# Kernel optimization log

Measured on AMD Instinct MI355X. Metric: run time of the kernel, lower is better.

The kernel has to match this reference:

```python
import jax, jax.numpy as jnp
import numpy as np

DOWNSAMPLE = 4
REG = 0.05
SINKHORN_ITERS = 50
LAMBDA_OT = 1.0
LAMBDA_TV = 1.0


def setup_inputs() -> dict:
    key = jax.random.key(0)
    k1, k2 = jax.random.split(key)
    pred = jax.random.uniform(k1, (16, 1, 256, 256), dtype=jnp.float32)
    gt = jax.random.uniform(k2, (16, 1, 256, 256), dtype=jnp.float32)
    return {"pred": pred, "gt": gt, "epoch": 5, "max_epoch": 10}


def _avg_pool(x, k):
    B, C, H, W = x.shape
    return x.reshape(B, C, H // k, k, W // k, k).mean(axis=(3, 5))


def _normalize(x, n):
    # relu then normalize to a distribution; fall back to uniform if sum==0
    x = jnp.maximum(x, 0.0)
    s = x.sum(axis=1, keepdims=True)  # [B,1]
    return jnp.where(s > 0, x / s, jnp.full_like(x, 1.0 / n))


def _curriculum_loss(pred, gt, epoch, max_epoch):
    B = pred.shape[0]
    # --- counting loss: L1 between total counts ---
    pc = pred.reshape(B, -1).sum(axis=1)
    gc = gt.reshape(B, -1).sum(axis=1)
    l_count = jnp.abs(pc - gc).mean()

    t = float(epoch) / float(max(1, max_epoch))
    ot_w = LAMBDA_OT * t
    tv_w = LAMBDA_TV * t

    # --- OT loss (batched Sinkhorn) ---
    pd = _avg_pool(pred, DOWNSAMPLE)
    gd = _avg_pool(gt, DOWNSAMPLE)
    h, w = pd.shape[2], pd.shape[3]
    n = h * w
    ys = jnp.arange(h, dtype=jnp.float32)
    xs = jnp.arange(w, dtype=jnp.float32)
    yy, xx = jnp.meshgrid(ys, xs, indexing="ij")
    yf = yy.reshape(-1)  # [n]
    xf = xx.reshape(-1)
    # squared euclidean cost matrix [n,n], built separably (no [n,n,2] temp)
    M = (yf[:, None] - yf[None, :]) ** 2 + (xf[:, None] - xf[None, :]) ** 2
    K = jnp.exp(-M / REG)  # [n,n]

    a = _normalize(pd.reshape(B, -1), n)  # [B,n]
    b = _normalize(gd.reshape(B, -1), n)

    def step(uv, _):
        u, v = uv
        u = a / (v @ K.T)  # K @ v per sample, batched
        v = b / (u @ K)    # K.T @ u per sample, batched
        return (u, v), None

    ones = jnp.ones((B, n), dtype=pred.dtype)
    (u, v), _ = jax.lax.scan(step, (ones, ones), None, length=SINKHORN_ITERS)
    # cost_b = sum_ij u_i K_ij v_j M_ij
    cost = jnp.einsum("bn,nm,bm->b", u, K * M, v)
    l_ot = cost.mean()

    # --- total variation loss ---
    dx = jnp.abs(pred[:, :, :, 1:] - pred[:, :, :, :-1]).mean()
    dy = jnp.abs(pred[:, :, 1:, :] - pred[:, :, :-1, :]).mean()
    l_tv = dx + dy

    return l_count + ot_w * l_ot + tv_w * l_tv


def reference(pred, gt, epoch, max_epoch):
    return _curriculum_loss(pred, gt, epoch, max_epoch)
```

## Files before the change

kernel.cpp:

```cpp
#include <hip/hip_runtime.h>
#include <math.h>


#define KW1 2.0611536224385578e-09f
#define MW2 8.4967085105831778e-18f
#define RP2 72
#define PDOFF 2048
#define GDOFF 67584

__device__ __forceinline__ float dpp_right(float x) {
  return __int_as_float(__builtin_amdgcn_update_dpp(
      0, __float_as_int(x), 0x101, 0xF, 0xF, true));
}
__device__ __forceinline__ float dpp_left(float x) {
  return __int_as_float(__builtin_amdgcn_update_dpp(
      0, __float_as_int(x), 0x111, 0xF, 0xF, true));
}
__device__ __forceinline__ float wshr1(float x) {
  return __int_as_float(__builtin_amdgcn_update_dpp(
      0, __float_as_int(x), 0x138, 0xF, 0xF, true));
}
__device__ __forceinline__ float wshl1(float x) {
  return __int_as_float(__builtin_amdgcn_update_dpp(
      0, __float_as_int(x), 0x130, 0xF, 0xF, true));
}

__device__ __forceinline__ float ad4(const float4 a, const float4 b) {
  return fabsf(a.x - b.x) + fabsf(a.y - b.y) + fabsf(a.z - b.z) + fabsf(a.w - b.w);
}
__device__ __forceinline__ float agent_ld(const float* p) {
  return __hip_atomic_load(p, __ATOMIC_RELAXED, __HIP_MEMORY_SCOPE_AGENT);
}

__global__ __launch_bounds__(256) void prep_kernel(
    const float* __restrict__ pred, const float* __restrict__ gt,
    float* __restrict__ ws) {
  __shared__ float rbuf[16];
  const int g = blockIdx.x;
  const int im = g >> 4, band = g & 15;
  const int t = threadIdx.x;
  const int ppy = t >> 6, ppx = t & 63;
  const float* pb = pred + im * 65536;
  const float* gb = gt + im * 65536;
  const int sr0 = band * 16 + ppy * 4;
  const int c0 = ppx * 4;

  float4 q[4];
  float ps = 0.f, gs = 0.f, sx = 0.f, sy = 0.f;
#pragma unroll
  for (int r = 0; r < 4; ++r) {
    q[r] = *(const float4*)(pb + (sr0 + r) * 256 + c0);
    const float4 e = *(const float4*)(gb + (sr0 + r) * 256 + c0);
    ps += (q[r].x + q[r].y) + (q[r].z + q[r].w);
    gs += (e.x + e.y) + (e.z + e.w);
    sx += fabsf(q[r].y - q[r].x) + fabsf(q[r].z - q[r].y) + fabsf(q[r].w - q[r].z);
    const float nf = __shfl_down(q[r].x, 1);
    if (ppx < 63) sx += fabsf(nf - q[r].w);
  }
  sy += ad4(q[1], q[0]) + ad4(q[2], q[1]) + ad4(q[3], q[2]);
  if (sr0 + 4 < 256) {
    const float4 qn = *(const float4*)(pb + (sr0 + 4) * 256 + c0);
    sy += ad4(qn, q[3]);
  }
  const int prow = band * 4 + ppy;
  ws[PDOFF + im * 4096 + prow * 64 + ppx] = fmaxf(ps * 0.0625f, 0.f);
  ws[GDOFF + im * 4096 + prow * 64 + ppx] = fmaxf(gs * 0.0625f, 0.f);

  float r0 = ps, r1 = gs, r2 = sx, r3 = sy;
#pragma unroll
  for (int o = 32; o > 0; o >>= 1) {
    r0 += __shfl_down(r0, o); r1 += __shfl_down(r1, o);
    r2 += __shfl_down(r2, o); r3 += __shfl_down(r3, o);
  }
  if ((t & 63) == 0) {
    const int w = t >> 6;
    rbuf[w * 4 + 0] = r0; rbuf[w * 4 + 1] = r1;
    rbuf[w * 4 + 2] = r2; rbuf[w * 4 + 3] = r3;
  }
  __syncthreads();
  if (t == 0) {
    float a0 = 0, a1 = 0, a2 = 0, a3 = 0;
    for (int w = 0; w < 4; ++w) {
      a0 += rbuf[w * 4]; a1 += rbuf[w * 4 + 1];
      a2 += rbuf[w * 4 + 2]; a3 += rbuf[w * 4 + 3];
    }
    ws[g] = a0; ws[256 + g] = a1; ws[512 + g] = a2; ws[768 + g] = a3;
  }
}

__global__ __launch_bounds__(256) void sink_kernel(
    float* __restrict__ ws, const int* __restrict__ epoch,
    const int* __restrict__ max_epoch, float* __restrict__ out,
    unsigned int* __restrict__ cnt) {
  __shared__ float SuL[6 * 64], SuR[6 * 64], SvL[6 * 64], SvR[6 * 64];
  __shared__ float rbuf[24];
  __shared__ int lastflag;

  const int b = blockIdx.x;
  const int t = threadIdx.x;
  const int w = t >> 6;
  const int l = t & 63;

  for (int i = t; i < 6 * 64; i += 256) {
    SuL[i] = 0.f; SuR[i] = 0.f; SvL[i] = 0.f; SvR[i] = 0.f;
  }
  __syncthreads();
  SvL[(w + 1) * 64 + l] = 1.f;
  SvR[(w + 1) * 64 + l] = 1.f;

  float av[16], bv[16];
  {
    const float* P = &ws[PDOFF + b * 4096 + l * 64 + w * 16];
    const float* G = &ws[GDOFF + b * 4096 + l * 64 + w * 16];
    float spd = 0.f, sgd = 0.f;
#pragma unroll
    for (int c4 = 0; c4 < 4; ++c4) {
      const float4 qa = *(const float4*)(P + 4 * c4);
      av[4 * c4] = qa.x; av[4 * c4 + 1] = qa.y;
      av[4 * c4 + 2] = qa.z; av[4 * c4 + 3] = qa.w;
      spd += (qa.x + qa.y) + (qa.z + qa.w);
      const float4 qb = *(const float4*)(G + 4 * c4);
      bv[4 * c4] = qb.x; bv[4 * c4 + 1] = qb.y;
      bv[4 * c4 + 2] = qb.z; bv[4 * c4 + 3] = qb.w;
      sgd += (qb.x + qb.y) + (qb.z + qb.w);
    }
#pragma unroll
    for (int o = 32; o > 0; o >>= 1) {
      spd += __shfl_down(spd, o); sgd += __shfl_down(sgd, o);
    }
    if (l == 0) { rbuf[w * 2] = spd; rbuf[w * 2 + 1] = sgd; }
  }
  __syncthreads();
  const float Sp = rbuf[0] + rbuf[2] + rbuf[4] + rbuf[6];
  const float Sg = rbuf[1] + rbuf[3] + rbuf[5] + rbuf[7];
#pragma unroll
  for (int c = 0; c < 16; ++c) {
    av[c] = (Sp > 0.f) ? (av[c] / Sp) : (1.f / 4096.f);
    bv[c] = (Sg > 0.f) ? (bv[c] / Sg) : (1.f / 4096.f);
  }

  const int rdL = w * 64 + l;
  const int rdR = (w + 2) * 64 + l;
  const int wr  = (w + 1) * 64 + l;

  float uu[16], vv[16], hh[16];
#pragma unroll
  for (int c = 0; c < 16; ++c) vv[c] = 1.f;
  __syncthreads();

#pragma unroll 1
  for (int it = 0; it < 50; ++it) {
    {
      const float xl = SvR[rdL];
      const float xr = SvL[rdR];
      hh[0] = fmaf(KW1, xl + vv[1], vv[0]);
#pragma unroll
      for (int c = 1; c < 15; ++c) hh[c] = fmaf(KW1, vv[c - 1] + vv[c + 1], vv[c]);
      hh[15] = fmaf(KW1, vv[14] + xr, vv[15]);
#pragma unroll
      for (int c = 0; c < 16; ++c) {
        const float up = wshr1(hh[c]);
        const float dn = wshl1(hh[c]);
        uu[c] = av[c] * __builtin_amdgcn_rcpf(fmaf(KW1, up + dn, hh[c]));
      }
      SuL[wr] = uu[0]; SuR[wr] = uu[15];
    }
    __syncthreads();
    {
      const float xl = SuR[rdL];
      const float xr = SuL[rdR];
      hh[0] = fmaf(KW1, xl + uu[1], uu[0]);
#pragma unroll
      for (int c = 1; c < 15; ++c) hh[c] = fmaf(KW1, uu[c - 1] + uu[c + 1], uu[c]);
      hh[15] = fmaf(KW1, uu[14] + xr, uu[15]);
#pragma unroll
      for (int c = 0; c < 16; ++c) {
        const float up = wshr1(hh[c]);
        const float dn = wshl1(hh[c]);
        vv[c] = bv[c] * __builtin_amdgcn_rcpf(fmaf(KW1, up + dn, hh[c]));
      }
      SvL[wr] = vv[0]; SvR[wr] = vv[15];
    }
    __syncthreads();
  }

  float c = 0.f;
  {
    const float xl = SvR[rdL];
    const float xr = SvL[rdR];
#pragma unroll
    for (int cc = 0; cc < 16; ++cc) {
      const float vl = (cc == 0) ? xl : vv[cc - 1];
      const float vr = (cc == 15) ? xr : vv[cc + 1];
      const float s = vl + vr;
      const float e = (wshr1(vv[cc]) + wshl1(vv[cc])) + s;
      const float d = wshr1(s) + wshl1(s);
      c += uu[cc] * fmaf(MW2, d, KW1 * e);
    }
  }
#pragma unroll
  for (int o = 32; o > 0; o >>= 1) c += __shfl_down(c, o);
  if (l == 0) rbuf[8 + w] = c;
  __syncthreads();
  if (t == 0) {
    ws[1024 + b] = rbuf[8] + rbuf[9] + rbuf[10] + rbuf[11];
    __threadfence();
    const unsigned int old = atomicAdd(cnt, 1u);
    lastflag = (old == 15u) ? 1 : 0;
  }
  __syncthreads();

  if (lastflag) {
    __threadfence();
    float myPc = agent_ld(&ws[t]);
    float myGc = agent_ld(&ws[256 + t]);
    float myTx = agent_ld(&ws[512 + t]);
    float myTy = agent_ld(&ws[768 + t]);
#pragma unroll
    for (int o = 8; o > 0; o >>= 1) {
      myPc += __shfl_down(myPc, o, 16);
      myGc += __shfl_down(myGc, o, 16);
    }
    float d = ((t & 15) == 0) ? fabsf(myPc - myGc) : 0.f;
    float ct = (t < 16) ? agent_ld(&ws[1024 + t]) : 0.f;
#pragma unroll
    for (int o = 32; o > 0; o >>= 1) {
      d += __shfl_down(d, o); ct += __shfl_down(ct, o);
      myTx += __shfl_down(myTx, o); myTy += __shfl_down(myTy, o);
    }
    if ((t & 63) == 0) {
      const int ww = t >> 6;
      rbuf[ww * 4] = d; rbuf[ww * 4 + 1] = ct;
      rbuf[ww * 4 + 2] = myTx; rbuf[ww * 4 + 3] = myTy;
    }
    __syncthreads();
    if (t == 0) {
      float lc = 0, lot = 0, tvx = 0, tvy = 0;
      for (int ww = 0; ww < 4; ++ww) {
        lc += rbuf[ww * 4]; lot += rbuf[ww * 4 + 1];
        tvx += rbuf[ww * 4 + 2]; tvy += rbuf[ww * 4 + 3];
      }
      int me = max_epoch[0]; if (me < 1) me = 1;
      const float tt = (float)epoch[0] / (float)me;
      const float ltv = tvx / (16.f * 256.f * 255.f) + tvy / (16.f * 255.f * 256.f);
      out[0] = lc * (1.f / 16.f) + tt * (lot * (1.f / 16.f)) + tt * ltv;
    }
  }
}

#define SPW1 2.0611536224385578e-09f
__device__ __forceinline__ void hrow4(const float f[4], float h[4]) {
  const float l = dpp_left(f[3]);
  const float r = dpp_right(f[0]);
  h[0] = fmaf(KW1, l + f[1], f[0]);
  h[1] = fmaf(KW1, f[0] + f[2], f[1]);
  h[2] = fmaf(KW1, f[1] + f[3], f[2]);
  h[3] = fmaf(KW1, f[2] + r, f[3]);
}
__device__ __forceinline__ void phase_core(
    const float prev[4][4], float ph[4][4],
    const float cf0[4], const float cf3[4],
    float2 mA, float4 mB, float2 mC, float2 pA, float4 pB, float2 pC,
    float* __restrict__ RT_wr, float* __restrict__ RB_wr, int wb,
    float out0[4], float out3[4]) {
  hrow4(prev[0], ph[0]); hrow4(prev[1], ph[1]);
  hrow4(prev[2], ph[2]); hrow4(prev[3], ph[3]);
  float hm[4], hp[4];
  hm[0] = fmaf(KW1, mA.y + mB.y, mB.x);
  hm[1] = fmaf(KW1, mB.x + mB.z, mB.y);
  hm[2] = fmaf(KW1, mB.y + mB.w, mB.z);
  hm[3] = fmaf(KW1, mB.z + mC.x, mB.w);
  hp[0] = fmaf(KW1, pA.y + pB.y, pB.x);
  hp[1] = fmaf(KW1, pB.x + pB.z, pB.y);
  hp[2] = fmaf(KW1, pB.y + pB.w, pB.z);
  hp[3] = fmaf(KW1, pB.z + pC.x, pB.w);
#pragma unroll
  for (int j = 0; j < 4; ++j)
    out0[j] = cf0[j] * __builtin_amdgcn_rcpf(fmaf(KW1, hm[j] + ph[1][j], ph[0][j]));
#pragma unroll
  for (int j = 0; j < 4; ++j)
    out3[j] = cf3[j] * __builtin_amdgcn_rcpf(fmaf(KW1, ph[2][j] + hp[j], ph[3][j]));
  *(float4*)&RT_wr[wb] = make_float4(out0[0], out0[1], out0[2], out0[3]);
  *(float4*)&RB_wr[wb] = make_float4(out3[0], out3[1], out3[2], out3[3]);
}

__global__ __launch_bounds__(256) void fused_fallback(
    const float* __restrict__ pred, const float* __restrict__ gt,
    float* __restrict__ ws, const int* __restrict__ epoch,
    const int* __restrict__ max_epoch, float* __restrict__ out,
    unsigned int* __restrict__ cnt) {
  __shared__ float RTu[18 * RP2], RBu[18 * RP2];
  __shared__ float RTv[18 * RP2], RBv[18 * RP2];
  __shared__ float rbuf[24];

  const int b = blockIdx.x;
  const int t = threadIdx.x;
  const int tyg = t >> 4, tx = t & 15;
  const int y0 = tyg * 4, x0 = tx * 4;

  for (int i = t; i < 18 * RP2; i += 256) {
    RTu[i] = 0.f; RBu[i] = 0.f; RTv[i] = 0.f; RBv[i] = 0.f;
  }

  const float* pb = pred + b * 65536;
  const float* gb = gt + b * 65536;
  const int sr0 = 4 * y0, sc0 = 4 * x0;

  float pd[4][4], gd[4][4];
  float4 pr0, pr1, pr2, pr3;
  float spraw = 0.f, sgraw = 0.f, sx = 0.f, sy = 0.f;
#pragma unroll
  for (int i = 0; i < 4; ++i) {
    float a0 = 0.f, a1 = 0.f, a2 = 0.f, a3 = 0.f;
    float c0 = 0.f, c1 = 0.f, c2 = 0.f, c3 = 0.f;
#pragma unroll 1
    for (int rr = 0; rr < 4; ++rr) {
      const int r = i * 4 + rr;
      const float* prow = pb + (sr0 + r) * 256 + sc0;
      const float4 q0 = *(const float4*)(prow);
      const float4 q1 = *(const float4*)(prow + 4);
      const float4 q2 = *(const float4*)(prow + 8);
      const float4 q3 = *(const float4*)(prow + 12);
      const float s0 = (q0.x + q0.y) + (q0.z + q0.w);
      const float s1 = (q1.x + q1.y) + (q1.z + q1.w);
      const float s2 = (q2.x + q2.y) + (q2.z + q2.w);
      const float s3 = (q3.x + q3.y) + (q3.z + q3.w);
      a0 += s0; a1 += s1; a2 += s2; a3 += s3;
      spraw += (s0 + s1) + (s2 + s3);
      sx += fabsf(q0.y - q0.x) + fabsf(q0.z - q0.y) + fabsf(q0.w - q0.z)
          + fabsf(q1.x - q0.w)
          + fabsf(q1.y - q1.x) + fabsf(q1.z - q1.y) + fabsf(q1.w - q1.z)
          + fabsf(q2.x - q1.w)
          + fabsf(q2.y - q2.x) + fabsf(q2.z - q2.y) + fabsf(q2.w - q2.z)
          + fabsf(q3.x - q2.w)
          + fabsf(q3.y - q3.x) + fabsf(q3.z - q3.y) + fabsf(q3.w - q3.z);
      const float nf = dpp_right(q0.x);
      if (tx < 15) sx += fabsf(nf - q3.w);
      if (r > 0) sy += ad4(q0, pr0) + ad4(q1, pr1) + ad4(q2, pr2) + ad4(q3, pr3);
      pr0 = q0; pr1 = q1; pr2 = q2; pr3 = q3;
      const float* grow = gb + (sr0 + r) * 256 + sc0;
      const float4 g0 = *(const float4*)(grow);
      const float4 g1 = *(const float4*)(grow + 4);
      const float4 g2 = *(const float4*)(grow + 8);
      const float4 g3 = *(const float4*)(grow + 12);
      const float u0 = (g0.x + g0.y) + (g0.z + g0.w);
      const float u1 = (g1.x + g1.y) + (g1.z + g1.w);
      const float u2 = (g2.x + g2.y) + (g2.z + g2.w);
      const float u3 = (g3.x + g3.y) + (g3.z + g3.w);
      c0 += u0; c1 += u1; c2 += u2; c3 += u3;
      sgraw += (u0 + u1) + (u2 + u3);
    }
    pd[i][0] = a0; pd[i][1] = a1; pd[i][2] = a2; pd[i][3] = a3;
    gd[i][0] = c0; gd[i][1] = c1; gd[i][2] = c2; gd[i][3] = c3;
  }
  if (tyg < 15) {
    const float* prow = pb + (sr0 + 16) * 256 + sc0;
    sy += ad4(*(const float4*)(prow), pr0) + ad4(*(const float4*)(prow + 4), pr1)
        + ad4(*(const float4*)(prow + 8), pr2) + ad4(*(const float4*)(prow + 12), pr3);
  }

  float spd = 0.f, sgd = 0.f;
#pragma unroll
  for (int i = 0; i < 4; ++i)
#pragma unroll
    for (int j = 0; j < 4; ++j) {
      pd[i][j] = fmaxf(pd[i][j] * 0.0625f, 0.f); spd += pd[i][j];
      gd[i][j] = fmaxf(gd[i][j] * 0.0625f, 0.f); sgd += gd[i][j];
    }

  float r0 = spraw, r1 = sgraw, r2 = spd, r3 = sgd, r4 = sx, r5 = sy;
#pragma unroll
  for (int o = 32; o > 0; o >>= 1) {
    r0 += __shfl_down(r0, o); r1 += __shfl_down(r1, o);
    r2 += __shfl_down(r2, o); r3 += __shfl_down(r3, o);
    r4 += __shfl_down(r4, o); r5 += __shfl_down(r5, o);
  }
  if ((t & 63) == 0) {
    const int w = t >> 6;
    rbuf[w * 6 + 0] = r0; rbuf[w * 6 + 1] = r1; rbuf[w * 6 + 2] = r2;
    rbuf[w * 6 + 3] = r3; rbuf[w * 6 + 4] = r4; rbuf[w * 6 + 5] = r5;
  }
  __syncthreads();
  if (t == 0) {
    float a0 = 0, a1 = 0, a2 = 0, a3 = 0, a4 = 0, a5 = 0;
    for (int w = 0; w < 4; ++w) {
      a0 += rbuf[w * 6 + 0]; a1 += rbuf[w * 6 + 1]; a2 += rbuf[w * 6 + 2];
      a3 += rbuf[w * 6 + 3]; a4 += rbuf[w * 6 + 4]; a5 += rbuf[w * 6 + 5];
    }
    ws[b] = a0; ws[16 + b] = a1; ws[48 + b] = a4; ws[64 + b] = a5;
    rbuf[0] = a2; rbuf[1] = a3;
  }
  __syncthreads();
  const float Sp = rbuf[0], Sg = rbuf[1];

  float av[4][4], bv[4][4];
#pragma unroll
  for (int i = 0; i < 4; ++i)
#pragma unroll
    for (int j = 0; j < 4; ++j) {
      av[i][j] = (Sp > 0.f) ? (pd[i][j] / Sp) : (1.f / 4096.f);
      bv[i][j] = (Sg > 0.f) ? (gd[i][j] / Sg) : (1.f / 4096.f);
    }

  const int rbb = tyg * RP2 + x0 + 2;
  const int rtb = (tyg + 2) * RP2 + x0 + 2;
  const int wb  = (1 + tyg) * RP2 + 4 + x0;

  float uu[4][4], vv[4][4], uh[4][4], vh[4][4];
#pragma unroll
  for (int i = 0; i < 4; ++i)
#pragma unroll
    for (int j = 0; j < 4; ++j) vv[i][j] = 1.f;
  *(float4*)&RTv[wb] = make_float4(1.f, 1.f, 1.f, 1.f);
  *(float4*)&RBv[wb] = make_float4(1.f, 1.f, 1.f, 1.f);
  __syncthreads();

#pragma unroll 1
  for (int it = 0; it < 50; ++it) {
    {
      const float2 mA = *(const float2*)&RBv[rbb];
      const float4 mB = *(const float4*)&RBv[rbb + 2];
      const float2 mC = *(const float2*)&RBv[rbb + 6];
      const float2 pA = *(const float2*)&RTv[rtb];
      const float4 pB = *(const float4*)&RTv[rtb + 2];
      const float2 pC = *(const float2*)&RTv[rtb + 6];
      if (it != 0) {
#pragma unroll
        for (int j = 0; j < 4; ++j) {
          vv[1][j] = bv[1][j] * __builtin_amdgcn_rcpf(fmaf(KW1, uh[0][j] + uh[2][j], uh[1][j]));
          vv[2][j] = bv[2][j] * __builtin_amdgcn_rcpf(fmaf(KW1, uh[1][j] + uh[3][j], uh[2][j]));
        }
      }
      phase_core(vv, vh, av[0], av[3], mA, mB, mC, pA, pB, pC,
                 RTu, RBu, wb, uu[0], uu[3]);
    }
    __syncthreads();
    {
      const float2 mA = *(const float2*)&RBu[rbb];
      const float4 mB = *(const float4*)&RBu[rbb + 2];
      const float2 mC = *(const float2*)&RBu[rbb + 6];
      const float2 pA = *(const float2*)&RTu[rtb];
      const float4 pB = *(const float4*)&RTu[rtb + 2];
      const float2 pC = *(const float2*)&RTu[rtb + 6];
#pragma unroll
      for (int j = 0; j < 4; ++j) {
        uu[1][j] = av[1][j] * __builtin_amdgcn_rcpf(fmaf(KW1, vh[0][j] + vh[2][j], vh[1][j]));
        uu[2][j] = av[2][j] * __builtin_amdgcn_rcpf(fmaf(KW1, vh[1][j] + vh[3][j], vh[2][j]));
      }
      phase_core(uu, uh, bv[0], bv[3], mA, mB, mC, pA, pB, pC,
                 RTv, RBv, wb, vv[0], vv[3]);
    }
    __syncthreads();
  }
#pragma unroll
  for (int j = 0; j < 4; ++j) {
    vv[1][j] = bv[1][j] * __builtin_amdgcn_rcpf(fmaf(KW1, uh[0][j] + uh[2][j], uh[1][j]));
    vv[2][j] = bv[2][j] * __builtin_amdgcn_rcpf(fmaf(KW1, uh[1][j] + uh[3][j], uh[2][j]));
  }

  float c = 0.f;
  {
    const float2 mA = *(const float2*)&RBv[rbb];
    const float4 mB = *(const float4*)&RBv[rbb + 2];
    const float2 mC = *(const float2*)&RBv[rbb + 6];
    const float2 pA = *(const float2*)&RTv[rtb];
    const float4 pB = *(const float4*)&RTv[rtb + 2];
    const float2 pC = *(const float2*)&RTv[rtb + 6];
    float W[6][6];
    W[0][0] = mA.y; W[0][1] = mB.x; W[0][2] = mB.y;
    W[0][3] = mB.z; W[0][4] = mB.w; W[0][5] = mC.x;
    W[5][0] = pA.y; W[5][1] = pB.x; W[5][2] = pB.y;
    W[5][3] = pB.z; W[5][4] = pB.w; W[5][5] = pC.x;
#pragma unroll
    for (int i = 0; i < 4; ++i) {
      W[1 + i][0] = dpp_left(vv[i][3]);
      W[1 + i][5] = dpp_right(vv[i][0]);
#pragma unroll
      for (int j = 0; j < 4; ++j) W[1 + i][1 + j] = vv[i][j];
    }
#pragma unroll
    for (int i = 0; i < 4; ++i)
#pragma unroll
      for (int j = 0; j < 4; ++j) {
        const float e = (W[i][j + 1] + W[i + 2][j + 1])
                      + (W[i + 1][j] + W[i + 1][j + 2]);
        const float d = (W[i][j] + W[i][j + 2])
                      + (W[i + 2][j] + W[i + 2][j + 2]);
        c += uu[i][j] * fmaf(MW2, d, KW1 * e);
      }
  }
#pragma unroll
  for (int o = 32; o > 0; o >>= 1) c += __shfl_down(c, o);
  if ((t & 63) == 0) rbuf[t >> 6] = c;
  __syncthreads();
  if (t == 0) {
    ws[32 + b] = rbuf[0] + rbuf[1] + rbuf[2] + rbuf[3];
    __threadfence();
    const unsigned int old = atomicAdd(cnt, 1u);
    if (old == 15u) {
      __threadfence();
      float lc = 0.f, lot = 0.f, tvx = 0.f, tvy = 0.f;
      for (int k = 0; k < 16; ++k) {
        const float p = agent_ld(&ws[k]);
        const float g = agent_ld(&ws[16 + k]);
        const float ct = agent_ld(&ws[32 + k]);
        const float x = agent_ld(&ws[48 + k]);
        const float y = agent_ld(&ws[64 + k]);
        lc += fabsf(p - g); lot += ct; tvx += x; tvy += y;
      }
      int me = max_epoch[0]; if (me < 1) me = 1;
      const float tt = (float)epoch[0] / (float)me;
      const float ltv = tvx / (16.f * 256.f * 255.f) + tvy / (16.f * 255.f * 256.f);
      out[0] = lc * (1.f / 16.f) + tt * (lot * (1.f / 16.f)) + tt * ltv;
    }
  }
}

extern "C" void kernel_launch(void* const* d_in, const int* in_sizes, int n_in,
                              void* d_out, int out_size, void* d_ws, size_t ws_size,
                              hipStream_t stream) {
  const float* pred = (const float*)d_in[0];
  const float* gt   = (const float*)d_in[1];
  const int* epoch  = (const int*)d_in[2];
  const int* max_ep = (const int*)d_in[3];
  float* out = (float*)d_out;
  float* ws  = (float*)d_ws;

  if (ws_size >= 600000) {
    unsigned int* cnt = (unsigned int*)((char*)d_ws + 4160);
    hipMemsetAsync(cnt, 0, 4, stream);
    prep_kernel<<<dim3(256), dim3(256), 0, stream>>>(pred, gt, ws);
    sink_kernel<<<dim3(16), dim3(256), 0, stream>>>(ws, epoch, max_ep, out, cnt);
  } else {
    unsigned int* cnt = (unsigned int*)((char*)d_ws + 384);
    hipMemsetAsync(cnt, 0, 4, stream);
    fused_fallback<<<dim3(16), dim3(256), 0, stream>>>(pred, gt, ws, epoch,
                                                       max_ep, out, cnt);
  }
}
```

Before: 103.9 us.

## Use 4-column halos so Sinkhorn waves exchange boundaries every two iterations

Each wave now keeps 24 columns in registers: its own 16 plus a 4-column halo on each side. It runs four half-steps (two Sinkhorn iterations), letting the valid region shrink by one column per half-step, and only then swaps halos through shared memory. That replaces two barriers per iteration with one barrier per two iterations, and the shared buffers are double-buffered so a single sync is enough. The cost is extra redundant arithmetic and more registers per thread, plus a clamp on the denominator to avoid dividing by zero in halo columns outside the field.

```diff
diff --git a/kernel.cpp b/kernel.cpp
--- a/kernel.cpp
+++ b/kernel.cpp
@@ -30,6 +30,20 @@
 }
 __device__ __forceinline__ float agent_ld(const float* p) {
   return __hip_atomic_load(p, __ATOMIC_RELAXED, __HIP_MEMORY_SCOPE_AGENT);
+}
+
+template <int LO, int HI>
+__device__ __forceinline__ void half_phase(const float (&src)[24],
+                                           const float (&cf)[24],
+                                           float (&dst)[24], float (&hh)[24]) {
+#pragma unroll
+  for (int i = LO; i <= HI; ++i)
+    hh[i] = fmaf(KW1, src[i - 1] + src[i + 1], src[i]);
+#pragma unroll
+  for (int i = LO; i <= HI; ++i) {
+    const float d = fmaf(KW1, wshr1(hh[i]) + wshl1(hh[i]), hh[i]);
+    dst[i] = cf[i] * __builtin_amdgcn_rcpf(fmaxf(d, 1e-30f));
+  }
 }
 
 __global__ __launch_bounds__(256) void prep_kernel(
@@ -92,7 +106,7 @@
     float* __restrict__ ws, const int* __restrict__ epoch,
     const int* __restrict__ max_epoch, float* __restrict__ out,
     unsigned int* __restrict__ cnt) {
-  __shared__ float SuL[6 * 64], SuR[6 * 64], SvL[6 * 64], SvR[6 * 64];
+  __shared__ float SL[2][6 * 256], SR[2][6 * 256];
   __shared__ float rbuf[24];
   __shared__ int lastflag;
 
@@ -100,103 +114,76 @@
   const int t = threadIdx.x;
   const int w = t >> 6;
   const int l = t & 63;
-
-  for (int i = t; i < 6 * 64; i += 256) {
-    SuL[i] = 0.f; SuR[i] = 0.f; SvL[i] = 0.f; SvR[i] = 0.f;
-  }
-  __syncthreads();
-  SvL[(w + 1) * 64 + l] = 1.f;
-  SvR[(w + 1) * 64 + l] = 1.f;
-
-  float av[16], bv[16];
-  {
-    const float* P = &ws[PDOFF + b * 4096 + l * 64 + w * 16];
-    const float* G = &ws[GDOFF + b * 4096 + l * 64 + w * 16];
-    float spd = 0.f, sgd = 0.f;
-#pragma unroll
-    for (int c4 = 0; c4 < 4; ++c4) {
-      const float4 qa = *(const float4*)(P + 4 * c4);
-      av[4 * c4] = qa.x; av[4 * c4 + 1] = qa.y;
-      av[4 * c4 + 2] = qa.z; av[4 * c4 + 3] = qa.w;
-      spd += (qa.x + qa.y) + (qa.z + qa.w);
-      const float4 qb = *(const float4*)(G + 4 * c4);
-      bv[4 * c4] = qb.x; bv[4 * c4 + 1] = qb.y;
-      bv[4 * c4 + 2] = qb.z; bv[4 * c4 + 3] = qb.w;
-      sgd += (qb.x + qb.y) + (qb.z + qb.w);
-    }
-#pragma unroll
-    for (int o = 32; o > 0; o >>= 1) {
-      spd += __shfl_down(spd, o); sgd += __shfl_down(sgd, o);
-    }
-    if (l == 0) { rbuf[w * 2] = spd; rbuf[w * 2 + 1] = sgd; }
-  }
+  const int colbase = 16 * w - 4;
+
+  for (int i = t; i < 6 * 256; i += 256) {
+    SL[0][i] = 0.f; SR[0][i] = 0.f; SL[1][i] = 0.f; SR[1][i] = 0.f;
+  }
+
+  float av[24], bv[24];
+  const float* P = &ws[PDOFF + b * 4096 + l * 64];
+  const float* G = &ws[GDOFF + b * 4096 + l * 64];
+#pragma unroll
+  for (int k = 0; k < 6; ++k) {
+    const int c0 = colbase + 4 * k;
+    if (c0 >= 0 && c0 <= 60) {
+      const float4 qa = *(const float4*)(P + c0);
+      av[4 * k] = qa.x; av[4 * k + 1] = qa.y;
+      av[4 * k + 2] = qa.z; av[4 * k + 3] = qa.w;
+      const float4 qb = *(const float4*)(G + c0);
+      bv[4 * k] = qb.x; bv[4 * k + 1] = qb.y;
+      bv[4 * k + 2] = qb.z; bv[4 * k + 3] = qb.w;
+    } else {
+      av[4 * k] = 0.f; av[4 * k + 1] = 0.f; av[4 * k + 2] = 0.f; av[4 * k + 3] = 0.f;
+      bv[4 * k] = 0.f; bv[4 * k + 1] = 0.f; bv[4 * k + 2] = 0.f; bv[4 * k + 3] = 0.f;
+    }
+  }
+  float spd = 0.f, sgd = 0.f;
+#pragma unroll
+  for (int i = 4; i < 20; ++i) { spd += av[i]; sgd += bv[i]; }
+#pragma unroll
+  for (int o = 32; o > 0; o >>= 1) {
+    spd += __shfl_down(spd, o); sgd += __shfl_down(sgd, o);
+  }
+  if (l == 0) { rbuf[w * 2] = spd; rbuf[w * 2 + 1] = sgd; }
   __syncthreads();
   const float Sp = rbuf[0] + rbuf[2] + rbuf[4] + rbuf[6];
   const float Sg = rbuf[1] + rbuf[3] + rbuf[5] + rbuf[7];
-#pragma unroll
-  for (int c = 0; c < 16; ++c) {
-    av[c] = (Sp > 0.f) ? (av[c] / Sp) : (1.f / 4096.f);
-    bv[c] = (Sg > 0.f) ? (bv[c] / Sg) : (1.f / 4096.f);
-  }
-
-  const int rdL = w * 64 + l;
-  const int rdR = (w + 2) * 64 + l;
-  const int wr  = (w + 1) * 64 + l;
-
-  float uu[16], vv[16], hh[16];
-#pragma unroll
-  for (int c = 0; c < 16; ++c) vv[c] = 1.f;
-  __syncthreads();
+
+  float vv[24], uu[24], hh[24];
+#pragma unroll
+  for (int i = 0; i < 24; ++i) {
+    const bool infld = (unsigned)(colbase + i) < 64u;
+    av[i] = infld ? ((Sp > 0.f) ? (av[i] / Sp) : (1.f / 4096.f)) : 0.f;
+    bv[i] = infld ? ((Sg > 0.f) ? (bv[i] / Sg) : (1.f / 4096.f)) : 0.f;
+    vv[i] = infld ? 1.f : 0.f;
+    uu[i] = 0.f; hh[i] = 0.f;
+  }
 
 #pragma unroll 1
-  for (int it = 0; it < 50; ++it) {
-    {
-      const float xl = SvR[rdL];
-      const float xr = SvL[rdR];
-      hh[0] = fmaf(KW1, xl + vv[1], vv[0]);
-#pragma unroll
-      for (int c = 1; c < 15; ++c) hh[c] = fmaf(KW1, vv[c - 1] + vv[c + 1], vv[c]);
-      hh[15] = fmaf(KW1, vv[14] + xr, vv[15]);
-#pragma unroll
-      for (int c = 0; c < 16; ++c) {
-        const float up = wshr1(hh[c]);
-        const float dn = wshl1(hh[c]);
-        uu[c] = av[c] * __builtin_amdgcn_rcpf(fmaf(KW1, up + dn, hh[c]));
-      }
-      SuL[wr] = uu[0]; SuR[wr] = uu[15];
-    }
+  for (int p = 0; p < 25; ++p) {
+    half_phase<1, 22>(vv, av, uu, hh);
+    half_phase<2, 21>(uu, bv, vv, hh);
+    half_phase<3, 20>(vv, av, uu, hh);
+    half_phase<4, 19>(uu, bv, vv, hh);
+    float* sl = SL[p & 1];
+    float* sr = SR[p & 1];
+    *(float4*)&sl[(w + 1) * 256 + l * 4] = make_float4(vv[4], vv[5], vv[6], vv[7]);
+    *(float4*)&sr[(w + 1) * 256 + l * 4] = make_float4(vv[16], vv[17], vv[18], vv[19]);
     __syncthreads();
-    {
-      const float xl = SuR[rdL];
-      const float xr = SuL[rdR];
-      hh[0] = fmaf(KW1, xl + uu[1], uu[0]);
-#pragma unroll
-      for (int c = 1; c < 15; ++c) hh[c] = fmaf(KW1, uu[c - 1] + uu[c + 1], uu[c]);
-      hh[15] = fmaf(KW1, uu[14] + xr, uu[15]);
-#pragma unroll
-      for (int c = 0; c < 16; ++c) {
-        const float up = wshr1(hh[c]);
-        const float dn = wshl1(hh[c]);
-        vv[c] = bv[c] * __builtin_amdgcn_rcpf(fmaf(KW1, up + dn, hh[c]));
-      }
-      SvL[wr] = vv[0]; SvR[wr] = vv[15];
-    }
-    __syncthreads();
+    const float4 Lh = *(const float4*)&sr[w * 256 + l * 4];
+    const float4 Rh = *(const float4*)&sl[(w + 2) * 256 + l * 4];
+    vv[0] = Lh.x; vv[1] = Lh.y; vv[2] = Lh.z; vv[3] = Lh.w;
+    vv[20] = Rh.x; vv[21] = Rh.y; vv[22] = Rh.z; vv[23] = Rh.w;
   }
 
   float c = 0.f;
-  {
-    const float xl = SvR[rdL];
-    const float xr = SvL[rdR];
-#pragma unroll
-    for (int cc = 0; cc < 16; ++cc) {
-      const float vl = (cc == 0) ? xl : vv[cc - 1];
-      const float vr = (cc == 15) ? xr : vv[cc + 1];
-      const float s = vl + vr;
-      const float e = (wshr1(vv[cc]) + wshl1(vv[cc])) + s;
-      const float d = wshr1(s) + wshl1(s);
-      c += uu[cc] * fmaf(MW2, d, KW1 * e);
-    }
+#pragma unroll
+  for (int cc = 4; cc < 20; ++cc) {
+    const float s = vv[cc - 1] + vv[cc + 1];
+    const float e = (wshr1(vv[cc]) + wshl1(vv[cc])) + s;
+    const float d = wshr1(s) + wshl1(s);
+    c += uu[cc] * fmaf(MW2, d, KW1 * e);
   }
 #pragma unroll
   for (int o = 32; o > 0; o >>= 1) c += __shfl_down(c, o);
@@ -248,7 +235,6 @@
   }
 }
 
-#define SPW1 2.0611536224385578e-09f
 __device__ __forceinline__ void hrow4(const float f[4], float h[4]) {
   const float l = dpp_left(f[3]);
   const float r = dpp_right(f[0]);
```

Measured after the change: 106.0 us. +2.1%, slower.

## Widen Sinkhorn blocks to 1024 threads and fold counter reset into prep kernel

Applied to the files above, without the earlier changes.

The Sinkhorn kernel now runs each image with 16 waves of 1024 threads instead of 4 waves, so each thread holds 4 columns rather than 16. The shared halo buffers and reductions are resized to match. This shortens the serial per-thread work in each of the 50 iterations, at the cost of more expensive block-wide barriers. The separate memset that cleared the completion counter is removed, and prep_kernel's first thread zeroes it instead, which saves one launch.

```diff
diff --git a/kernel.cpp b/kernel.cpp
--- a/kernel.cpp
+++ b/kernel.cpp
@@ -34,11 +34,12 @@
 
 __global__ __launch_bounds__(256) void prep_kernel(
     const float* __restrict__ pred, const float* __restrict__ gt,
-    float* __restrict__ ws) {
+    float* __restrict__ ws, unsigned int* __restrict__ cnt) {
   __shared__ float rbuf[16];
   const int g = blockIdx.x;
   const int im = g >> 4, band = g & 15;
   const int t = threadIdx.x;
+  if (g == 0 && t == 0) *cnt = 0u;
   const int ppy = t >> 6, ppx = t & 63;
   const float* pb = pred + im * 65536;
   const float* gb = gt + im * 65536;
@@ -88,12 +89,12 @@
   }
 }
 
-__global__ __launch_bounds__(256) void sink_kernel(
+__global__ __launch_bounds__(1024) void sink_kernel(
     float* __restrict__ ws, const int* __restrict__ epoch,
     const int* __restrict__ max_epoch, float* __restrict__ out,
     unsigned int* __restrict__ cnt) {
-  __shared__ float SuL[6 * 64], SuR[6 * 64], SvL[6 * 64], SvR[6 * 64];
-  __shared__ float rbuf[24];
+  __shared__ float SuL[18 * 64], SuR[18 * 64], SvL[18 * 64], SvR[18 * 64];
+  __shared__ float rbuf[40];
   __shared__ int lastflag;
 
   const int b = blockIdx.x;
@@ -101,51 +102,39 @@
   const int w = t >> 6;
   const int l = t & 63;
 
-  for (int i = t; i < 6 * 64; i += 256) {
+  for (int i = t; i < 18 * 64; i += 1024) {
     SuL[i] = 0.f; SuR[i] = 0.f; SvL[i] = 0.f; SvR[i] = 0.f;
   }
-  __syncthreads();
-  SvL[(w + 1) * 64 + l] = 1.f;
-  SvR[(w + 1) * 64 + l] = 1.f;
-
-  float av[16], bv[16];
-  {
-    const float* P = &ws[PDOFF + b * 4096 + l * 64 + w * 16];
-    const float* G = &ws[GDOFF + b * 4096 + l * 64 + w * 16];
-    float spd = 0.f, sgd = 0.f;
-#pragma unroll
-    for (int c4 = 0; c4 < 4; ++c4) {
-      const float4 qa = *(const float4*)(P + 4 * c4);
-      av[4 * c4] = qa.x; av[4 * c4 + 1] = qa.y;
-      av[4 * c4 + 2] = qa.z; av[4 * c4 + 3] = qa.w;
-      spd += (qa.x + qa.y) + (qa.z + qa.w);
-      const float4 qb = *(const float4*)(G + 4 * c4);
-      bv[4 * c4] = qb.x; bv[4 * c4 + 1] = qb.y;
-      bv[4 * c4 + 2] = qb.z; bv[4 * c4 + 3] = qb.w;
-      sgd += (qb.x + qb.y) + (qb.z + qb.w);
-    }
-#pragma unroll
-    for (int o = 32; o > 0; o >>= 1) {
-      spd += __shfl_down(spd, o); sgd += __shfl_down(sgd, o);
-    }
-    if (l == 0) { rbuf[w * 2] = spd; rbuf[w * 2 + 1] = sgd; }
-  }
-  __syncthreads();
-  const float Sp = rbuf[0] + rbuf[2] + rbuf[4] + rbuf[6];
-  const float Sg = rbuf[1] + rbuf[3] + rbuf[5] + rbuf[7];
-#pragma unroll
-  for (int c = 0; c < 16; ++c) {
-    av[c] = (Sp > 0.f) ? (av[c] / Sp) : (1.f / 4096.f);
-    bv[c] = (Sg > 0.f) ? (bv[c] / Sg) : (1.f / 4096.f);
+
+  float av[4], bv[4];
+  const float4 qa = *(const float4*)&ws[PDOFF + b * 4096 + l * 64 + 4 * w];
+  const float4 qb = *(const float4*)&ws[GDOFF + b * 4096 + l * 64 + 4 * w];
+  av[0] = qa.x; av[1] = qa.y; av[2] = qa.z; av[3] = qa.w;
+  bv[0] = qb.x; bv[1] = qb.y; bv[2] = qb.z; bv[3] = qb.w;
+  float spd = (qa.x + qa.y) + (qa.z + qa.w);
+  float sgd = (qb.x + qb.y) + (qb.z + qb.w);
+#pragma unroll
+  for (int o = 32; o > 0; o >>= 1) {
+    spd += __shfl_down(spd, o); sgd += __shfl_down(sgd, o);
+  }
+  if (l == 0) { rbuf[w * 2] = spd; rbuf[w * 2 + 1] = sgd; }
+  __syncthreads();
+  float Sp = 0.f, Sg = 0.f;
+#pragma unroll
+  for (int k = 0; k < 16; ++k) { Sp += rbuf[2 * k]; Sg += rbuf[2 * k + 1]; }
+
+#pragma unroll
+  for (int j = 0; j < 4; ++j) {
+    av[j] = (Sp > 0.f) ? (av[j] / Sp) : (1.f / 4096.f);
+    bv[j] = (Sg > 0.f) ? (bv[j] / Sg) : (1.f / 4096.f);
   }
 
   const int rdL = w * 64 + l;
   const int rdR = (w + 2) * 64 + l;
   const int wr  = (w + 1) * 64 + l;
 
-  float uu[16], vv[16], hh[16];
-#pragma unroll
-  for (int c = 0; c < 16; ++c) vv[c] = 1.f;
+  float uu[4], vv[4] = {1.f, 1.f, 1.f, 1.f}, hh[4];
+  SvL[wr] = 1.f; SvR[wr] = 1.f;
   __syncthreads();
 
 #pragma unroll 1
@@ -154,32 +143,30 @@
       const float xl = SvR[rdL];
       const float xr = SvL[rdR];
       hh[0] = fmaf(KW1, xl + vv[1], vv[0]);
-#pragma unroll
-      for (int c = 1; c < 15; ++c) hh[c] = fmaf(KW1, vv[c - 1] + vv[c + 1], vv[c]);
-      hh[15] = fmaf(KW1, vv[14] + xr, vv[15]);
-#pragma unroll
-      for (int c = 0; c < 16; ++c) {
-        const float up = wshr1(hh[c]);
-        const float dn = wshl1(hh[c]);
-        uu[c] = av[c] * __builtin_amdgcn_rcpf(fmaf(KW1, up + dn, hh[c]));
-      }
-      SuL[wr] = uu[0]; SuR[wr] = uu[15];
+      hh[1] = fmaf(KW1, vv[0] + vv[2], vv[1]);
+      hh[2] = fmaf(KW1, vv[1] + vv[3], vv[2]);
+      hh[3] = fmaf(KW1, vv[2] + xr, vv[3]);
+#pragma unroll
+      for (int c = 0; c < 4; ++c) {
+        const float d = fmaf(KW1, wshr1(hh[c]) + wshl1(hh[c]), hh[c]);
+        uu[c] = av[c] * __builtin_amdgcn_rcpf(d);
+      }
+      SuL[wr] = uu[0]; SuR[wr] = uu[3];
     }
     __syncthreads();
     {
       const float xl = SuR[rdL];
       const float xr = SuL[rdR];
       hh[0] = fmaf(KW1, xl + uu[1], uu[0]);
-#pragma unroll
-      for (int c = 1; c < 15; ++c) hh[c] = fmaf(KW1, uu[c - 1] + uu[c + 1], uu[c]);
-      hh[15] = fmaf(KW1, uu[14] + xr, uu[15]);
-#pragma unroll
-      for (int c = 0; c < 16; ++c) {
-        const float up = wshr1(hh[c]);
-        const float dn = wshl1(hh[c]);
-        vv[c] = bv[c] * __builtin_amdgcn_rcpf(fmaf(KW1, up + dn, hh[c]));
-      }
-      SvL[wr] = vv[0]; SvR[wr] = vv[15];
+      hh[1] = fmaf(KW1, uu[0] + uu[2], uu[1]);
+      hh[2] = fmaf(KW1, uu[1] + uu[3], uu[2]);
+      hh[3] = fmaf(KW1, uu[2] + xr, uu[3]);
+#pragma unroll
+      for (int c = 0; c < 4; ++c) {
+        const float d = fmaf(KW1, wshr1(hh[c]) + wshl1(hh[c]), hh[c]);
+        vv[c] = bv[c] * __builtin_amdgcn_rcpf(d);
+      }
+      SvL[wr] = vv[0]; SvR[wr] = vv[3];
     }
     __syncthreads();
   }
@@ -189,9 +176,9 @@
     const float xl = SvR[rdL];
     const float xr = SvL[rdR];
 #pragma unroll
-    for (int cc = 0; cc < 16; ++cc) {
+    for (int cc = 0; cc < 4; ++cc) {
       const float vl = (cc == 0) ? xl : vv[cc - 1];
-      const float vr = (cc == 15) ? xr : vv[cc + 1];
+      const float vr = (cc == 3) ? xr : vv[cc + 1];
       const float s = vl + vr;
       const float e = (wshr1(vv[cc]) + wshl1(vv[cc])) + s;
       const float d = wshr1(s) + wshl1(s);
@@ -200,10 +187,12 @@
   }
 #pragma unroll
   for (int o = 32; o > 0; o >>= 1) c += __shfl_down(c, o);
-  if (l == 0) rbuf[8 + w] = c;
+  if (l == 0) rbuf[w] = c;
   __syncthreads();
   if (t == 0) {
-    ws[1024 + b] = rbuf[8] + rbuf[9] + rbuf[10] + rbuf[11];
+    float s = 0.f;
+    for (int k = 0; k < 16; ++k) s += rbuf[k];
+    ws[1024 + b] = s;
     __threadfence();
     const unsigned int old = atomicAdd(cnt, 1u);
     lastflag = (old == 15u) ? 1 : 0;
@@ -212,10 +201,13 @@
 
   if (lastflag) {
     __threadfence();
-    float myPc = agent_ld(&ws[t]);
-    float myGc = agent_ld(&ws[256 + t]);
-    float myTx = agent_ld(&ws[512 + t]);
-    float myTy = agent_ld(&ws[768 + t]);
+    float myPc = 0.f, myGc = 0.f, myTx = 0.f, myTy = 0.f;
+    if (t < 256) {
+      myPc = agent_ld(&ws[t]);
+      myGc = agent_ld(&ws[256 + t]);
+      myTx = agent_ld(&ws[512 + t]);
+      myTy = agent_ld(&ws[768 + t]);
+    }
 #pragma unroll
     for (int o = 8; o > 0; o >>= 1) {
       myPc += __shfl_down(myPc, o, 16);
@@ -228,17 +220,17 @@
       d += __shfl_down(d, o); ct += __shfl_down(ct, o);
       myTx += __shfl_down(myTx, o); myTy += __shfl_down(myTy, o);
     }
-    if ((t & 63) == 0) {
+    if ((t & 63) == 0 && t < 256) {
       const int ww = t >> 6;
-      rbuf[ww * 4] = d; rbuf[ww * 4 + 1] = ct;
-      rbuf[ww * 4 + 2] = myTx; rbuf[ww * 4 + 3] = myTy;
+      rbuf[16 + ww * 4] = d; rbuf[16 + ww * 4 + 1] = ct;
+      rbuf[16 + ww * 4 + 2] = myTx; rbuf[16 + ww * 4 + 3] = myTy;
     }
     __syncthreads();
     if (t == 0) {
       float lc = 0, lot = 0, tvx = 0, tvy = 0;
       for (int ww = 0; ww < 4; ++ww) {
-        lc += rbuf[ww * 4]; lot += rbuf[ww * 4 + 1];
-        tvx += rbuf[ww * 4 + 2]; tvy += rbuf[ww * 4 + 3];
+        lc += rbuf[16 + ww * 4]; lot += rbuf[16 + ww * 4 + 1];
+        tvx += rbuf[16 + ww * 4 + 2]; tvy += rbuf[16 + ww * 4 + 3];
       }
       int me = max_epoch[0]; if (me < 1) me = 1;
       const float tt = (float)epoch[0] / (float)me;
@@ -248,7 +240,6 @@
   }
 }
 
-#define SPW1 2.0611536224385578e-09f
 __device__ __forceinline__ void hrow4(const float f[4], float h[4]) {
   const float l = dpp_left(f[3]);
   const float r = dpp_right(f[0]);
@@ -528,9 +519,8 @@
 
   if (ws_size >= 600000) {
     unsigned int* cnt = (unsigned int*)((char*)d_ws + 4160);
-    hipMemsetAsync(cnt, 0, 4, stream);
-    prep_kernel<<<dim3(256), dim3(256), 0, stream>>>(pred, gt, ws);
-    sink_kernel<<<dim3(16), dim3(256), 0, stream>>>(ws, epoch, max_ep, out, cnt);
+    prep_kernel<<<dim3(256), dim3(256), 0, stream>>>(pred, gt, ws, cnt);
+    sink_kernel<<<dim3(16), dim3(1024), 0, stream>>>(ws, epoch, max_ep, out, cnt);
   } else {
     unsigned int* cnt = (unsigned int*)((char*)d_ws + 384);
     hipMemsetAsync(cnt, 0, 4, stream);
```

After: 100.3 us, median of 2. -3.5%, faster.
